# Kernel tuning notes

Measured on AMD Instinct MI355X. Metric: run time of the kernel, lower is better.

Reference implementation:

```python
import jax, jax.numpy as jnp
import numpy as np

B, N, K = 8, 2048, 4          # graphs per batch, nodes per graph, knn k
IN_CH, HID, C = 16, 128, 64   # in_channels, GCN hidden, n_clusters
E = 262144                    # input edges


def gcn_conv(x, src, dst, W, b):
    """PyG GCNConv: self-loops + symmetric normalization + linear."""
    n = x.shape[0]
    xw = x @ W
    loop = jnp.arange(n)
    s2 = jnp.concatenate([src, loop])
    d2 = jnp.concatenate([dst, loop])
    deg = jax.ops.segment_sum(jnp.ones(s2.shape[0], x.dtype), d2, num_segments=n)
    dis = jax.lax.rsqrt(deg)  # deg >= 1 thanks to self loops
    norm = dis[s2] * dis[d2]
    return jax.ops.segment_sum(xw[s2] * norm[:, None], d2, num_segments=n) + b


def knn_edges(coords):
    """knn_graph(k=K, loop=False) per graph; edges neighbor->node (source_to_target)."""
    c = coords.reshape(B, N, 3)
    d2 = jnp.sum((c[:, :, None, :] - c[:, None, :, :]) ** 2, -1)  # [B,N,N]
    d2 = d2 + jnp.eye(N, dtype=c.dtype) * jnp.asarray(1e10, c.dtype)  # exclude self
    _, idx = jax.lax.top_k(-d2, K)  # [B,N,K] local neighbor indices
    offs = (jnp.arange(B) * N)[:, None, None]
    src = (idx + offs).reshape(-1)
    dst = (jnp.broadcast_to(jnp.arange(N)[None, :, None], (B, N, K)) + offs).reshape(-1)
    return src, dst


def dmon_pool(x, adj, Wp, bp):
    """PyG DMoNPooling (eval mode, mask all-true since graphs are equal-sized)."""
    s = jax.nn.softmax(x @ Wp + bp, axis=-1)              # [B,N,C]
    out = jax.nn.selu(jnp.einsum('bnc,bnf->bcf', s, x))   # [B,C,F]
    out_adj = jnp.einsum('bnc,bnm,bmd->bcd', s, adj, s)   # [B,C,C]
    deg = adj.sum(1)                                      # column sums, [B,N]
    m = deg.sum(-1) / 2                                   # [B]
    ca = jnp.einsum('bnc,bn->bc', s, deg)                 # [B,C]
    normalizer = ca[:, :, None] * ca[:, None, :] / (2 * m)[:, None, None]
    spectral = (-jnp.trace(out_adj - normalizer, axis1=1, axis2=2) / (2 * m)).mean()
    ss = jnp.einsum('bnc,bnd->bcd', s, s)
    ss_fro = jnp.linalg.norm(ss, axis=(1, 2), keepdims=True)
    i_norm = jnp.sqrt(jnp.asarray(C, x.dtype))            # ||I_C||_F
    i_s = jnp.eye(C, dtype=x.dtype)
    ortho = jnp.linalg.norm(ss / ss_fro - i_s / i_norm, axis=(1, 2)).mean()
    cluster = (jnp.linalg.norm(s.sum(1), axis=1) / N * i_norm - 1).mean()
    return s, out, spectral, ortho, cluster


def forward(x, edge_src, edge_dst, W1, b1, W2, b2, Wp, bp):
    h = jax.nn.relu(gcn_conv(x, edge_src, edge_dst, W1, b1))
    src2, dst2 = knn_edges(h[:, :3])                      # dynamic graph on dims [0,1,2]
    h = jax.nn.relu(gcn_conv(h, src2, dst2, W2, b2))
    xd = h.reshape(B, N, HID)                             # to_dense_batch (equal-size graphs)
    g = edge_src // N                                     # to_dense_adj on ORIGINAL edges
    adj = jnp.zeros((B, N, N), x.dtype).at[g, edge_src % N, edge_dst % N].add(1.0)
    s, out, sp, o, cl = dmon_pool(xd, adj, Wp, bp)
    return jax.nn.log_softmax(out, axis=-1), sp + o + cl, s


def setup_inputs():
    key = jax.random.key(0)
    ks = jax.random.split(key, 8)
    x = jax.random.normal(ks[0], (B * N, IN_CH), jnp.float32)
    g = jax.random.randint(ks[1], (E,), 0, B)
    edge_src = (g * N + jax.random.randint(ks[2], (E,), 0, N)).astype(jnp.int32)
    edge_dst = (g * N + jax.random.randint(ks[3], (E,), 0, N)).astype(jnp.int32)
    batch = jnp.repeat(jnp.arange(B, dtype=jnp.int32), N)
    W1 = jax.random.normal(ks[4], (IN_CH, HID), jnp.float32) / np.sqrt(IN_CH)
    b1 = jnp.zeros((HID,), jnp.float32)
    W2 = jax.random.normal(ks[5], (HID, HID), jnp.float32) / np.sqrt(HID)
    b2 = jnp.zeros((HID,), jnp.float32)
    Wp = jax.random.normal(ks[6], (HID, C), jnp.float32) / np.sqrt(HID)
    bp = jnp.zeros((C,), jnp.float32)
    return {"x": x, "edge_src": edge_src, "edge_dst": edge_dst, "batch": batch,
            "W1": W1, "b1": b1, "W2": W2, "b2": b2, "Wp": Wp, "bp": bp}


def reference(x, edge_src, edge_dst, batch, W1, b1, W2, b2, Wp, bp):
    del batch  # graphs are equal-sized contiguous blocks of N nodes
    return forward(x, edge_src, edge_dst, W1, b1, W2, b2, Wp, bp)
```

## Files before the change

### kernel.cpp

```cpp
#include <hip/hip_runtime.h>
#include <math.h>

#define BGR 8
#define NN 2048
#define KNN 4
#define INCH 16
#define HID 128
#define CL 64
#define NE 262144
#define NT (BGR*NN)

#define OFF_CNT   0
#define OFF_CSR   16384
#define OFF_H1    1064960
#define OFF_NBR   3162112
#define OFF_SS    3227648
#define OFF_H2    4276224
#define OFF_TR    6373376
#define OFF_CA    6373384
#define OFF_SSUM  6373896
#define OFF_MS    6374408
#define OFF_H1C   6374416

__global__ void k_init(int* cnt, float* small, float* loss) {
  int i = blockIdx.x * 256 + threadIdx.x;
  if (i < 16384) cnt[i] = 0;
  int j = i - 16384;
  if (j >= 0 && j < 1040) small[j] = 0.f;
  if (i == 0) loss[0] = 0.f;
}

__global__ void k_bucket(const int* __restrict__ src, const int* __restrict__ dst,
                         int* __restrict__ cnt, int* __restrict__ csr) {
  int e = blockIdx.x * 256 + threadIdx.x;
  if (e >= NE) return;
  int d = dst[e];
  int slot = atomicAdd(&cnt[d], 1);
  if (slot < 64) csr[(d << 6) + slot] = src[e];
}

__global__ __launch_bounds__(256) void k_gemm1(const int* __restrict__ cnt,
    const int* __restrict__ csr, const float* __restrict__ x,
    const float* __restrict__ W1, const float* __restrict__ b1,
    float* __restrict__ h1, float* __restrict__ h1c) {
  __shared__ float a1[16][17];
  __shared__ float w[INCH * HID];
  __shared__ float disl[NN];
  int tid = threadIdx.x;
  int gbase = (blockIdx.x >> 7) * NN;
  for (int i = tid; i < NN; i += 256)
    disl[i] = rsqrtf((float)cnt[gbase + i] + 1.0f);
  for (int i = tid; i < INCH * HID / 4; i += 256) ((float4*)w)[i] = ((const float4*)W1)[i];
  int nl = tid >> 4, ch = tid & 15;
  int n = blockIdx.x * 16 + nl;
  int cnRaw = cnt[n];
  int cn = cnRaw > 64 ? 64 : cnRaw;
  const int* row = csr + (n << 6);
  __syncthreads();
  float dn = disl[n - gbase];
  float acc = 0.f;
  int sNext = (cn > 0) ? row[0] : 0;
  for (int e = 0; e < cn; e++) {
    int sc = sNext;
    if (e + 1 < cn) sNext = row[e + 1];
    acc += x[sc * INCH + ch] * disl[sc - gbase];
  }
  a1[nl][ch] = (acc + x[n * INCH + ch] * dn) * dn;
  __syncthreads();
  int j = tid & 127;
  int ng = (tid >> 7) * 8;
#pragma unroll
  for (int u = 0; u < 8; u++) {
    int node = ng + u;
    float s = b1[j];
#pragma unroll
    for (int c2 = 0; c2 < INCH; c2++) s += a1[node][c2] * w[c2 * HID + j];
    float v = fmaxf(s, 0.f);
    h1[(size_t)(blockIdx.x * 16 + node) * HID + j] = v;
    if (j < 4) h1c[(size_t)(blockIdx.x * 16 + node) * 4 + j] = v;
  }
}

__global__ __launch_bounds__(1024) void k_knn(const float* __restrict__ h1c, int* __restrict__ nbr) {
  __shared__ float4 c4[NN];
  int g = blockIdx.y, tid = threadIdx.x;
  const float4* src4 = (const float4*)h1c + (size_t)g * NN;
  for (int i = tid; i < NN; i += 1024) c4[i] = src4[i];
  __syncthreads();
  int wid = tid >> 6, lane = tid & 63;
  int row0 = blockIdx.x * 32 + wid * 2;
  float mx[2], my[2], mz[2];
#pragma unroll
  for (int r = 0; r < 2; r++) { float4 m = c4[row0 + r]; mx[r] = m.x; my[r] = m.y; mz[r] = m.z; }
  unsigned t0[2], t1[2], t2[2], t3[2];
#pragma unroll
  for (int r = 0; r < 2; r++) { t0[r] = t1[r] = t2[r] = t3[r] = 0xFFFFFFFFu; }
#pragma unroll 4
  for (int i = 0; i < 32; i++) {
    int j = i * 64 + lane;
    float4 p = c4[j];
#pragma unroll
    for (int r = 0; r < 2; r++) {
      float dx = p.x - mx[r], dy = p.y - my[r], dz = p.z - mz[r];
      float d2 = dx * dx + dy * dy + dz * dz;
      unsigned k = (__float_as_uint(d2) & 0xFFFFFFE0u) | (unsigned)i;
      if (j == row0 + r) k = 0xFFFFFFFFu;
      unsigned M0 = max(t0[r], k); t0[r] = min(t0[r], k);
      unsigned M1 = max(t1[r], M0); t1[r] = min(t1[r], M0);
      unsigned M2 = max(t2[r], M1); t2[r] = min(t2[r], M1);
      t3[r] = min(t3[r], M2);
    }
  }
#pragma unroll
  for (int r = 0; r < 2; r++) {
    unsigned a0 = t0[r], a1 = t1[r], a2 = t2[r], a3 = t3[r];
    int res[4];
#pragma unroll
    for (int k = 0; k < 4; k++) {
      int cj = (int)((a0 & 31u) << 6) | lane;
      unsigned wd = a0; int wj = cj;
#pragma unroll
      for (int off = 32; off; off >>= 1) {
        unsigned od = (unsigned)__shfl_xor((int)wd, off, 64);
        int oj = __shfl_xor(wj, off, 64);
        bool take = (od < wd) || (od == wd && oj < wj);
        wd = take ? od : wd; wj = take ? oj : wj;
      }
      res[k] = wj;
      bool pop = (cj == wj);
      a0 = pop ? a1 : a0; a1 = pop ? a2 : a1; a2 = pop ? a3 : a2;
      a3 = pop ? 0xFFFFFFFFu : a3;
    }
    if (lane == 0) {
      int node = g * NN + row0 + r;
      ((int4*)nbr)[node] = make_int4(g * NN + res[0], g * NN + res[1],
                                     g * NN + res[2], g * NN + res[3]);
    }
  }
}

__global__ __launch_bounds__(256) void k_gemm2s(const float* __restrict__ h1,
    const int* __restrict__ nbr, const float* __restrict__ W2,
    const float* __restrict__ b2, const float* __restrict__ Wp,
    const float* __restrict__ bp, float* __restrict__ h2,
    float* __restrict__ s_out) {
  __shared__ float smem[13344];
  float (*At)[33] = (float(*)[33])smem;
  float* Bt = smem + 1056;
  float (*H2t)[128] = (float(*)[128])smem;
  float* Wpl = smem + 5152;
  int tid = threadIdx.x;
  int bid = blockIdx.x;
  int rblock = (bid & 7) * 64 + (bid >> 3);
  int rbase = rblock * 32;
  int r = tid >> 3, q = tid & 7;
  int4 nb = ((const int4*)nbr)[rbase + r];
  const float4* h4 = (const float4*)h1;
  size_t r0 = (size_t)(rbase + r) * 32, rx = (size_t)nb.x * 32, ry = (size_t)nb.y * 32,
         rz = (size_t)nb.z * 32, rw = (size_t)nb.w * 32;
  int rg = tid >> 5;
  int cg = (tid & 31) * 4;
  float acc[4][4];
#pragma unroll
  for (int i = 0; i < 4; i++)
#pragma unroll
    for (int j = 0; j < 4; j++) acc[i][j] = 0.f;
  int kk = tid >> 5;
  int cc = (tid & 31) * 4;
  for (int k0 = 0; k0 < HID; k0 += 32) {
    {
      int q4 = (k0 >> 2) + q;
      float4 a = h4[r0 + q4], bx = h4[rx + q4], by = h4[ry + q4],
             bz = h4[rz + q4], bw = h4[rw + q4];
      int k = q * 4;
      At[r][k]     = (a.x + bx.x + by.x + bz.x + bw.x) * 0.2f;
      At[r][k + 1] = (a.y + bx.y + by.y + bz.y + bw.y) * 0.2f;
      At[r][k + 2] = (a.z + bx.z + by.z + bz.z + bw.z) * 0.2f;
      At[r][k + 3] = (a.w + bx.w + by.w + bz.w + bw.w) * 0.2f;
    }
#pragma unroll
    for (int u = 0; u < 4; u++)
      *(float4*)&Bt[(kk + u * 8) * 128 + cc] = *(const float4*)&W2[(k0 + kk + u * 8) * HID + cc];
    {
      int kt = k0 >> 5;
      *(float4*)&Wpl[kt * 2048 + tid * 8]     = *(const float4*)&Wp[kt * 2048 + tid * 8];
      *(float4*)&Wpl[kt * 2048 + tid * 8 + 4] = *(const float4*)&Wp[kt * 2048 + tid * 8 + 4];
    }
    __syncthreads();
#pragma unroll
    for (int k2 = 0; k2 < 32; k2++) {
      float4 bv = *(const float4*)&Bt[k2 * 128 + cg];
#pragma unroll
      for (int i = 0; i < 4; i++) {
        float av = At[rg * 4 + i][k2];
        acc[i][0] += av * bv.x; acc[i][1] += av * bv.y;
        acc[i][2] += av * bv.z; acc[i][3] += av * bv.w;
      }
    }
    __syncthreads();
  }
#pragma unroll
  for (int i = 0; i < 4; i++) {
    int rr = rbase + rg * 4 + i;
#pragma unroll
    for (int j = 0; j < 4; j++) {
      float v = acc[i][j] + b2[cg + j];
      v = fmaxf(v, 0.f);
      h2[(size_t)rr * HID + cg + j] = v;
      H2t[rg * 4 + i][cg + j] = v;
    }
  }
  __syncthreads();
  int c0 = (tid & 31) * 2;
  float acc2[4][2];
  float bp0 = bp[c0], bp1 = bp[c0 + 1];
#pragma unroll
  for (int i = 0; i < 4; i++) { acc2[i][0] = bp0; acc2[i][1] = bp1; }
#pragma unroll 4
  for (int k2 = 0; k2 < 128; k2++) {
    float w0 = Wpl[k2 * 64 + c0];
    float w1 = Wpl[k2 * 64 + c0 + 1];
#pragma unroll
    for (int i = 0; i < 4; i++) {
      float av = H2t[rg * 4 + i][k2];
      acc2[i][0] += av * w0; acc2[i][1] += av * w1;
    }
  }
#pragma unroll
  for (int i = 0; i < 4; i++) {
    float m = fmaxf(acc2[i][0], acc2[i][1]);
    for (int off = 1; off < 32; off <<= 1) m = fmaxf(m, __shfl_xor(m, off, 64));
    float e0 = expf(acc2[i][0] - m), e1 = expf(acc2[i][1] - m);
    float sum = e0 + e1;
    for (int off = 1; off < 32; off <<= 1) sum += __shfl_xor(sum, off, 64);
    float inv = 1.0f / sum;
    size_t o = (size_t)(rbase + rg * 4 + i) * CL + c0;
    s_out[o] = e0 * inv;
    s_out[o + 1] = e1 * inv;
  }
}

__global__ __launch_bounds__(256) void k_dmon_trace(const float* __restrict__ s,
    const float* __restrict__ h2, const int* __restrict__ cnt,
    float* __restrict__ part_pool, float* __restrict__ part_ss,
    float* __restrict__ ca, float* __restrict__ ssum, float* __restrict__ msum,
    const int* __restrict__ src, const int* __restrict__ dst, float* __restrict__ tr) {
  __shared__ float st[64 * 64];
  __shared__ float ht[64 * 128];
  __shared__ float dt[64];
  __shared__ float red[256];
  __shared__ float bins[8];
  int tid = threadIdx.x;
  if (blockIdx.x < 256) {
    int b = blockIdx.x & 7, sl = blockIdx.x >> 3;
    int nb = sl * 64;
    const float* sp = s + ((size_t)b * NN + nb) * CL;
    const float* hp = h2 + ((size_t)b * NN + nb) * HID;
    for (int i = tid; i < 64 * 64 / 4; i += 256) ((float4*)st)[i] = ((const float4*)sp)[i];
    for (int i = tid; i < 64 * 128 / 4; i += 256) ((float4*)ht)[i] = ((const float4*)hp)[i];
    if (tid < 64) dt[tid] = (float)cnt[b * NN + nb + tid];
    __syncthreads();
    int tc = tid & 15, tf = tid >> 4;
    int c0 = tc * 4, f0 = tf * 8;
    float pacc[4][8];
#pragma unroll
    for (int i = 0; i < 4; i++)
#pragma unroll
      for (int j = 0; j < 8; j++) pacc[i][j] = 0.f;
    for (int n = 0; n < 64; n++) {
      float4 sv = *(const float4*)&st[n * 64 + c0];
      float4 ha = *(const float4*)&ht[n * 128 + f0];
      float4 hb = *(const float4*)&ht[n * 128 + f0 + 4];
      float svv[4] = {sv.x, sv.y, sv.z, sv.w};
#pragma unroll
      for (int i = 0; i < 4; i++) {
        pacc[i][0] += svv[i] * ha.x; pacc[i][1] += svv[i] * ha.y;
        pacc[i][2] += svv[i] * ha.z; pacc[i][3] += svv[i] * ha.w;
        pacc[i][4] += svv[i] * hb.x; pacc[i][5] += svv[i] * hb.y;
        pacc[i][6] += svv[i] * hb.z; pacc[i][7] += svv[i] * hb.w;
      }
    }
    float* pp = part_pool + ((size_t)(b * 32 + sl)) * 8192;
#pragma unroll
    for (int i = 0; i < 4; i++) {
      *(float4*)&pp[(c0 + i) * 128 + f0]     = make_float4(pacc[i][0], pacc[i][1], pacc[i][2], pacc[i][3]);
      *(float4*)&pp[(c0 + i) * 128 + f0 + 4] = make_float4(pacc[i][4], pacc[i][5], pacc[i][6], pacc[i][7]);
    }
    int d0 = tf * 4;
    float sacc[4][4];
#pragma unroll
    for (int i = 0; i < 4; i++)
#pragma unroll
      for (int j = 0; j < 4; j++) sacc[i][j] = 0.f;
    for (int n = 0; n < 64; n++) {
      float4 a = *(const float4*)&st[n * 64 + c0];
      float4 bq = *(const float4*)&st[n * 64 + d0];
      float av[4] = {a.x, a.y, a.z, a.w};
#pragma unroll
      for (int i = 0; i < 4; i++) {
        sacc[i][0] += av[i] * bq.x; sacc[i][1] += av[i] * bq.y;
        sacc[i][2] += av[i] * bq.z; sacc[i][3] += av[i] * bq.w;
      }
    }
    float* ps = part_ss + ((size_t)(b * 32 + sl)) * 4096;
#pragma unroll
    for (int i = 0; i < 4; i++)
      *(float4*)&ps[(c0 + i) * 64 + d0] = make_float4(sacc[i][0], sacc[i][1], sacc[i][2], sacc[i][3]);
    int c = tid & 63;
    int q = tid >> 6;
    float a_ss = 0, a_ca = 0, a_m = 0;
    for (int n = q; n < 64; n += 4) {
      float sv = st[n * 64 + c];
      float dv = dt[n];
      a_ss += sv; a_ca += sv * dv;
      if (c == 0) a_m += dv;
    }
    red[tid] = a_ss; __syncthreads();
    if (q == 0) atomicAdd(&ssum[b * CL + c], red[c] + red[64 + c] + red[128 + c] + red[192 + c]);
    __syncthreads();
    red[tid] = a_ca; __syncthreads();
    if (q == 0) atomicAdd(&ca[b * CL + c], red[c] + red[64 + c] + red[128 + c] + red[192 + c]);
    __syncthreads();
    red[tid] = (c == 0) ? a_m : 0.f; __syncthreads();
    if (tid == 0) atomicAdd(&msum[b], red[0] + red[64] + red[128] + red[192]);
  } else {
    if (tid < 8) bins[tid] = 0.f;
    __syncthreads();
    int sub = tid & 15;
    int grp = ((blockIdx.x - 256) * 256 + tid) >> 4;
    const float4* s4 = (const float4*)s;
    for (int e = grp; e < NE; e += 8192) {
      int se = src[e], de = dst[e];
      float4 a = s4[se * 16 + sub];
      float4 b = s4[de * 16 + sub];
      float v = a.x * b.x + a.y * b.y + a.z * b.z + a.w * b.w;
      v += __shfl_xor(v, 1, 64);
      v += __shfl_xor(v, 2, 64);
      v += __shfl_xor(v, 4, 64);
      v += __shfl_xor(v, 8, 64);
      if (sub == 0) atomicAdd(&bins[se >> 11], v);
    }
    __syncthreads();
    if (tid < 8) atomicAdd(&tr[tid], bins[tid]);
  }
}

__global__ __launch_bounds__(256) void k_final(const float* __restrict__ part_pool,
    const float* __restrict__ part_ss, const float* __restrict__ ca,
    const float* __restrict__ ssum, const float* __restrict__ msum,
    const float* __restrict__ tr, float* __restrict__ out, float* __restrict__ outs) {
  int tid = threadIdx.x;
  if (blockIdx.x < 256) {
    __shared__ float r[4], r2[4];
    int half = tid >> 7, f = tid & 127;
    int row = blockIdx.x * 2 + half;
    int wid = tid >> 6;
    const float* p = part_pool + (size_t)(row >> 6) * 32 * 8192 + (row & 63) * 128 + f;
    float v = 0.f;
#pragma unroll
    for (int sl = 0; sl < 32; sl++) v += p[sl * 8192];
    const float scale = 1.0507009873554805f, alpha = 1.6732632423543772f;
    v = scale * (v > 0.f ? v : alpha * expm1f(v));
    float m = v;
    for (int off = 32; off; off >>= 1) m = fmaxf(m, __shfl_xor(m, off, 64));
    if ((tid & 63) == 0) r[wid] = m;
    __syncthreads();
    m = fmaxf(r[half * 2], r[half * 2 + 1]);
    float e = expf(v - m);
    float sum = e;
    for (int off = 32; off; off >>= 1) sum += __shfl_xor(sum, off, 64);
    if ((tid & 63) == 0) r2[wid] = sum;
    __syncthreads();
    sum = r2[half * 2] + r2[half * 2 + 1];
    out[(size_t)row * HID + f] = v - m - logf(sum);
  } else {
    __shared__ float ssb[4096];
    __shared__ float red[256];
    int b = blockIdx.x - 256;
    float loc = 0.f;
    for (int idx = tid; idx < 4096; idx += 256) {
      const float* p = part_ss + (size_t)b * 32 * 4096 + idx;
      float v = 0.f;
#pragma unroll
      for (int sl = 0; sl < 32; sl++) v += p[sl * 4096];
      ssb[idx] = v;
      loc += v * v;
    }
    red[tid] = loc; __syncthreads();
    for (int s2 = 128; s2; s2 >>= 1) { if (tid < s2) red[tid] += red[tid + s2]; __syncthreads(); }
    float fro = sqrtf(red[0]);
    __syncthreads();
    loc = 0.f;
    for (int i = tid; i < 4096; i += 256) {
      float v = ssb[i] / fro - (((i % 65) == 0) ? 0.125f : 0.f);
      loc += v * v;
    }
    red[tid] = loc; __syncthreads();
    for (int s2 = 128; s2; s2 >>= 1) { if (tid < s2) red[tid] += red[tid + s2]; __syncthreads(); }
    float ortho_b = sqrtf(red[0]);
    __syncthreads();
    loc = 0.f;
    if (tid < 64) { float v = ca[b * 64 + tid]; loc = v * v; }
    red[tid] = loc; __syncthreads();
    for (int s2 = 128; s2; s2 >>= 1) { if (tid < s2) red[tid] += red[tid + s2]; __syncthreads(); }
    float caSq = red[0];
    __syncthreads();
    loc = 0.f;
    if (tid < 64) { float v = ssum[b * 64 + tid]; loc = v * v; }
    red[tid] = loc; __syncthreads();
    for (int s2 = 128; s2; s2 >>= 1) { if (tid < s2) red[tid] += red[tid + s2]; __syncthreads(); }
    float ssumSq = red[0];
    __syncthreads();
    if (tid == 0) {
      float m2 = msum[b];
      float spectral_b = -(tr[b] - caSq / m2) / m2;
      float cluster_b = sqrtf(ssumSq) / 2048.0f * 8.0f - 1.0f;
      atomicAdd(&outs[0], (spectral_b + ortho_b + cluster_b) * 0.125f);
    }
  }
}

extern "C" void kernel_launch(void* const* d_in, const int* in_sizes, int n_in,
                              void* d_out, int out_size, void* d_ws, size_t ws_size,
                              hipStream_t stream) {
  (void)in_sizes; (void)n_in; (void)out_size; (void)ws_size;
  const float* x   = (const float*)d_in[0];
  const int* esrc  = (const int*)d_in[1];
  const int* edst  = (const int*)d_in[2];
  const float* W1  = (const float*)d_in[4];
  const float* b1  = (const float*)d_in[5];
  const float* W2  = (const float*)d_in[6];
  const float* b2  = (const float*)d_in[7];
  const float* Wp  = (const float*)d_in[8];
  const float* bp  = (const float*)d_in[9];
  float* out = (float*)d_out;
  float* ws  = (float*)d_ws;

  int*   cnt   = (int*)(ws + OFF_CNT);
  int*   csr   = (int*)(ws + OFF_CSR);
  float* h1    = ws + OFF_H1;
  int*   nbr   = (int*)(ws + OFF_NBR);
  float* h2    = ws + OFF_H2;
  float* tr    = ws + OFF_TR;
  float* ca    = ws + OFF_CA;
  float* ssum  = ws + OFF_SSUM;
  float* msum  = ws + OFF_MS;
  float* h1c   = ws + OFF_H1C;
  float* part_pool = ws + OFF_H1;
  float* part_ss   = ws + OFF_SS;
  float* s_out = out + 65537;

  k_init<<<69, 256, 0, stream>>>(cnt, ws + OFF_TR, out + 65536);
  k_bucket<<<NE / 256, 256, 0, stream>>>(esrc, edst, cnt, csr);
  k_gemm1<<<NT / 16, 256, 0, stream>>>(cnt, csr, x, W1, b1, h1, h1c);
  k_knn<<<dim3(64, 8), 1024, 0, stream>>>(h1c, nbr);
  k_gemm2s<<<NT / 32, 256, 0, stream>>>(h1, nbr, W2, b2, Wp, bp, h2, s_out);
  k_dmon_trace<<<768, 256, 0, stream>>>(s_out, h2, cnt, part_pool, part_ss,
                                        ca, ssum, msum, esrc, edst, tr);
  k_final<<<264, 256, 0, stream>>>(part_pool, part_ss, ca, ssum, msum, tr,
                                   out, out + 65536);
}
```

Before: 197.1 us.

## Fuse kNN search with GCN2 gemm and pooling softmax into one kernel

```diff
diff --git a/kernel.cpp b/kernel.cpp
--- a/kernel.cpp
+++ b/kernel.cpp
@@ -13,7 +13,6 @@
 #define OFF_CNT   0
 #define OFF_CSR   16384
 #define OFF_H1    1064960
-#define OFF_NBR   3162112
 #define OFF_SS    3227648
 #define OFF_H2    4276224
 #define OFF_TR    6373376
@@ -81,163 +80,135 @@
   }
 }
 
-__global__ __launch_bounds__(1024) void k_knn(const float* __restrict__ h1c, int* __restrict__ nbr) {
-  __shared__ float4 c4[NN];
-  int g = blockIdx.y, tid = threadIdx.x;
+__global__ __launch_bounds__(1024) void k_kgs(const float* __restrict__ h1,
+    const float* __restrict__ h1c, const float* __restrict__ W2,
+    const float* __restrict__ b2, const float* __restrict__ Wp,
+    const float* __restrict__ bp, float* __restrict__ h2,
+    float* __restrict__ s_out) {
+  __shared__ float smem[8448];
+  __shared__ int4 nbrL[32];
+  int tid = threadIdx.x;
+  int bid = blockIdx.x;
+  int g = bid & 7, lb = bid >> 3;
+  int rbase = g * NN + lb * 32;
+
+  float4* c4 = (float4*)smem;
   const float4* src4 = (const float4*)h1c + (size_t)g * NN;
   for (int i = tid; i < NN; i += 1024) c4[i] = src4[i];
   __syncthreads();
   int wid = tid >> 6, lane = tid & 63;
-  int row0 = blockIdx.x * 32 + wid * 2;
-  float mx[2], my[2], mz[2];
-#pragma unroll
-  for (int r = 0; r < 2; r++) { float4 m = c4[row0 + r]; mx[r] = m.x; my[r] = m.y; mz[r] = m.z; }
-  unsigned t0[2], t1[2], t2[2], t3[2];
-#pragma unroll
-  for (int r = 0; r < 2; r++) { t0[r] = t1[r] = t2[r] = t3[r] = 0xFFFFFFFFu; }
+  int row0 = lb * 32 + wid * 2;
+  {
+    float mx[2], my[2], mz[2];
+#pragma unroll
+    for (int r = 0; r < 2; r++) { float4 m = c4[row0 + r]; mx[r] = m.x; my[r] = m.y; mz[r] = m.z; }
+    unsigned t0[2], t1[2], t2[2], t3[2];
+#pragma unroll
+    for (int r = 0; r < 2; r++) { t0[r] = t1[r] = t2[r] = t3[r] = 0xFFFFFFFFu; }
 #pragma unroll 4
-  for (int i = 0; i < 32; i++) {
-    int j = i * 64 + lane;
-    float4 p = c4[j];
+    for (int i = 0; i < 32; i++) {
+      int j = i * 64 + lane;
+      float4 p = c4[j];
+#pragma unroll
+      for (int r = 0; r < 2; r++) {
+        float dx = p.x - mx[r], dy = p.y - my[r], dz = p.z - mz[r];
+        float d2 = dx * dx + dy * dy + dz * dz;
+        unsigned k = (__float_as_uint(d2) & 0xFFFFFFE0u) | (unsigned)i;
+        if (j == row0 + r) k = 0xFFFFFFFFu;
+        unsigned M0 = max(t0[r], k); t0[r] = min(t0[r], k);
+        unsigned M1 = max(t1[r], M0); t1[r] = min(t1[r], M0);
+        unsigned M2 = max(t2[r], M1); t2[r] = min(t2[r], M1);
+        t3[r] = min(t3[r], M2);
+      }
+    }
 #pragma unroll
     for (int r = 0; r < 2; r++) {
-      float dx = p.x - mx[r], dy = p.y - my[r], dz = p.z - mz[r];
-      float d2 = dx * dx + dy * dy + dz * dz;
-      unsigned k = (__float_as_uint(d2) & 0xFFFFFFE0u) | (unsigned)i;
-      if (j == row0 + r) k = 0xFFFFFFFFu;
-      unsigned M0 = max(t0[r], k); t0[r] = min(t0[r], k);
-      unsigned M1 = max(t1[r], M0); t1[r] = min(t1[r], M0);
-      unsigned M2 = max(t2[r], M1); t2[r] = min(t2[r], M1);
-      t3[r] = min(t3[r], M2);
-    }
-  }
-#pragma unroll
-  for (int r = 0; r < 2; r++) {
-    unsigned a0 = t0[r], a1 = t1[r], a2 = t2[r], a3 = t3[r];
-    int res[4];
-#pragma unroll
-    for (int k = 0; k < 4; k++) {
-      int cj = (int)((a0 & 31u) << 6) | lane;
-      unsigned wd = a0; int wj = cj;
-#pragma unroll
-      for (int off = 32; off; off >>= 1) {
-        unsigned od = (unsigned)__shfl_xor((int)wd, off, 64);
-        int oj = __shfl_xor(wj, off, 64);
-        bool take = (od < wd) || (od == wd && oj < wj);
-        wd = take ? od : wd; wj = take ? oj : wj;
+      unsigned a0 = t0[r], a1 = t1[r], a2 = t2[r], a3 = t3[r];
+      int res[4];
+#pragma unroll
+      for (int k = 0; k < 4; k++) {
+        int cj = (int)((a0 & 31u) << 6) | lane;
+        unsigned wd = a0; int wj = cj;
+#pragma unroll
+        for (int off = 32; off; off >>= 1) {
+          unsigned od = (unsigned)__shfl_xor((int)wd, off, 64);
+          int oj = __shfl_xor(wj, off, 64);
+          bool take = (od < wd) || (od == wd && oj < wj);
+          wd = take ? od : wd; wj = take ? oj : wj;
+        }
+        res[k] = wj;
+        bool pop = (cj == wj);
+        a0 = pop ? a1 : a0; a1 = pop ? a2 : a1; a2 = pop ? a3 : a2;
+        a3 = pop ? 0xFFFFFFFFu : a3;
       }
-      res[k] = wj;
-      bool pop = (cj == wj);
-      a0 = pop ? a1 : a0; a1 = pop ? a2 : a1; a2 = pop ? a3 : a2;
-      a3 = pop ? 0xFFFFFFFFu : a3;
-    }
-    if (lane == 0) {
-      int node = g * NN + row0 + r;
-      ((int4*)nbr)[node] = make_int4(g * NN + res[0], g * NN + res[1],
-                                     g * NN + res[2], g * NN + res[3]);
-    }
-  }
-}
-
-__global__ __launch_bounds__(256) void k_gemm2s(const float* __restrict__ h1,
-    const int* __restrict__ nbr, const float* __restrict__ W2,
-    const float* __restrict__ b2, const float* __restrict__ Wp,
-    const float* __restrict__ bp, float* __restrict__ h2,
-    float* __restrict__ s_out) {
-  __shared__ float smem[13344];
-  float (*At)[33] = (float(*)[33])smem;
-  float* Bt = smem + 1056;
+      if (lane == 0)
+        nbrL[wid * 2 + r] = make_int4(g * NN + res[0], g * NN + res[1],
+                                      g * NN + res[2], g * NN + res[3]);
+    }
+  }
+  __syncthreads();
+
+  float (*At)[132] = (float(*)[132])smem;
+  float* Bt = smem + 4224;
+  const float4* h4 = (const float4*)h1;
+  int row = tid >> 5, q = tid & 31;
+  {
+    int4 nb = nbrL[row];
+    size_t r0 = (size_t)(rbase + row) * 32;
+    float4 a  = h4[r0 + q];
+    float4 bx = h4[(size_t)nb.x * 32 + q];
+    float4 by = h4[(size_t)nb.y * 32 + q];
+    float4 bz = h4[(size_t)nb.z * 32 + q];
+    float4 bw = h4[(size_t)nb.w * 32 + q];
+    At[row][q * 4]     = (a.x + bx.x + by.x + bz.x + bw.x) * 0.2f;
+    At[row][q * 4 + 1] = (a.y + bx.y + by.y + bz.y + bw.y) * 0.2f;
+    At[row][q * 4 + 2] = (a.z + bx.z + by.z + bz.z + bw.z) * 0.2f;
+    At[row][q * 4 + 3] = (a.w + bx.w + by.w + bz.w + bw.w) * 0.2f;
+  }
+  int cg = q * 4;
+  float acc[4] = {0.f, 0.f, 0.f, 0.f};
+  for (int kt = 0; kt < 4; kt++) {
+    *(float4*)&Bt[row * 128 + cg] = *(const float4*)&W2[(kt * 32 + row) * HID + cg];
+    __syncthreads();
+#pragma unroll
+    for (int k2 = 0; k2 < 32; k2++) {
+      float av = At[row][kt * 32 + k2];
+      float4 bv = *(const float4*)&Bt[k2 * 128 + cg];
+      acc[0] += av * bv.x; acc[1] += av * bv.y;
+      acc[2] += av * bv.z; acc[3] += av * bv.w;
+    }
+    __syncthreads();
+  }
+  float4 b2v = *(const float4*)&b2[cg];
+  float4 hv = make_float4(fmaxf(acc[0] + b2v.x, 0.f), fmaxf(acc[1] + b2v.y, 0.f),
+                          fmaxf(acc[2] + b2v.z, 0.f), fmaxf(acc[3] + b2v.w, 0.f));
+  *(float4*)&h2[(size_t)(rbase + row) * HID + cg] = hv;
+
   float (*H2t)[128] = (float(*)[128])smem;
-  float* Wpl = smem + 5152;
-  int tid = threadIdx.x;
-  int bid = blockIdx.x;
-  int rblock = (bid & 7) * 64 + (bid >> 3);
-  int rbase = rblock * 32;
-  int r = tid >> 3, q = tid & 7;
-  int4 nb = ((const int4*)nbr)[rbase + r];
-  const float4* h4 = (const float4*)h1;
-  size_t r0 = (size_t)(rbase + r) * 32, rx = (size_t)nb.x * 32, ry = (size_t)nb.y * 32,
-         rz = (size_t)nb.z * 32, rw = (size_t)nb.w * 32;
-  int rg = tid >> 5;
-  int cg = (tid & 31) * 4;
-  float acc[4][4];
-#pragma unroll
-  for (int i = 0; i < 4; i++)
-#pragma unroll
-    for (int j = 0; j < 4; j++) acc[i][j] = 0.f;
-  int kk = tid >> 5;
-  int cc = (tid & 31) * 4;
-  for (int k0 = 0; k0 < HID; k0 += 32) {
-    {
-      int q4 = (k0 >> 2) + q;
-      float4 a = h4[r0 + q4], bx = h4[rx + q4], by = h4[ry + q4],
-             bz = h4[rz + q4], bw = h4[rw + q4];
-      int k = q * 4;
-      At[r][k]     = (a.x + bx.x + by.x + bz.x + bw.x) * 0.2f;
-      At[r][k + 1] = (a.y + bx.y + by.y + bz.y + bw.y) * 0.2f;
-      At[r][k + 2] = (a.z + bx.z + by.z + bz.z + bw.z) * 0.2f;
-      At[r][k + 3] = (a.w + bx.w + by.w + bz.w + bw.w) * 0.2f;
-    }
-#pragma unroll
-    for (int u = 0; u < 4; u++)
-      *(float4*)&Bt[(kk + u * 8) * 128 + cc] = *(const float4*)&W2[(k0 + kk + u * 8) * HID + cc];
-    {
-      int kt = k0 >> 5;
-      *(float4*)&Wpl[kt * 2048 + tid * 8]     = *(const float4*)&Wp[kt * 2048 + tid * 8];
-      *(float4*)&Wpl[kt * 2048 + tid * 8 + 4] = *(const float4*)&Wp[kt * 2048 + tid * 8 + 4];
-    }
+  float* Wt = smem + 4096;
+  *(float4*)&H2t[row][cg] = hv;
+  int c0 = q * 2;
+  float acc2[2] = {bp[c0], bp[c0 + 1]};
+  for (int kt = 0; kt < 4; kt++) {
+    if (tid < 512) *(float4*)&Wt[tid * 4] = *(const float4*)&Wp[kt * 2048 + tid * 4];
     __syncthreads();
 #pragma unroll
     for (int k2 = 0; k2 < 32; k2++) {
-      float4 bv = *(const float4*)&Bt[k2 * 128 + cg];
-#pragma unroll
-      for (int i = 0; i < 4; i++) {
-        float av = At[rg * 4 + i][k2];
-        acc[i][0] += av * bv.x; acc[i][1] += av * bv.y;
-        acc[i][2] += av * bv.z; acc[i][3] += av * bv.w;
-      }
-    }
-    __syncthreads();
-  }
-#pragma unroll
-  for (int i = 0; i < 4; i++) {
-    int rr = rbase + rg * 4 + i;
-#pragma unroll
-    for (int j = 0; j < 4; j++) {
-      float v = acc[i][j] + b2[cg + j];
-      v = fmaxf(v, 0.f);
-      h2[(size_t)rr * HID + cg + j] = v;
-      H2t[rg * 4 + i][cg + j] = v;
-    }
-  }
-  __syncthreads();
-  int c0 = (tid & 31) * 2;
-  float acc2[4][2];
-  float bp0 = bp[c0], bp1 = bp[c0 + 1];
-#pragma unroll
-  for (int i = 0; i < 4; i++) { acc2[i][0] = bp0; acc2[i][1] = bp1; }
-#pragma unroll 4
-  for (int k2 = 0; k2 < 128; k2++) {
-    float w0 = Wpl[k2 * 64 + c0];
-    float w1 = Wpl[k2 * 64 + c0 + 1];
-#pragma unroll
-    for (int i = 0; i < 4; i++) {
-      float av = H2t[rg * 4 + i][k2];
-      acc2[i][0] += av * w0; acc2[i][1] += av * w1;
-    }
-  }
-#pragma unroll
-  for (int i = 0; i < 4; i++) {
-    float m = fmaxf(acc2[i][0], acc2[i][1]);
-    for (int off = 1; off < 32; off <<= 1) m = fmaxf(m, __shfl_xor(m, off, 64));
-    float e0 = expf(acc2[i][0] - m), e1 = expf(acc2[i][1] - m);
-    float sum = e0 + e1;
-    for (int off = 1; off < 32; off <<= 1) sum += __shfl_xor(sum, off, 64);
-    float inv = 1.0f / sum;
-    size_t o = (size_t)(rbase + rg * 4 + i) * CL + c0;
-    s_out[o] = e0 * inv;
-    s_out[o + 1] = e1 * inv;
-  }
+      float av = H2t[row][kt * 32 + k2];
+      acc2[0] += av * Wt[k2 * 64 + c0];
+      acc2[1] += av * Wt[k2 * 64 + c0 + 1];
+    }
+    __syncthreads();
+  }
+  float m = fmaxf(acc2[0], acc2[1]);
+  for (int off = 1; off < 32; off <<= 1) m = fmaxf(m, __shfl_xor(m, off, 64));
+  float e0 = expf(acc2[0] - m), e1 = expf(acc2[1] - m);
+  float sum = e0 + e1;
+  for (int off = 1; off < 32; off <<= 1) sum += __shfl_xor(sum, off, 64);
+  float inv = 1.0f / sum;
+  size_t o = (size_t)(rbase + row) * CL + c0;
+  s_out[o] = e0 * inv;
+  s_out[o + 1] = e1 * inv;
 }
 
 __global__ __launch_bounds__(256) void k_dmon_trace(const float* __restrict__ s,
@@ -439,7 +410,6 @@
   int*   cnt   = (int*)(ws + OFF_CNT);
   int*   csr   = (int*)(ws + OFF_CSR);
   float* h1    = ws + OFF_H1;
-  int*   nbr   = (int*)(ws + OFF_NBR);
   float* h2    = ws + OFF_H2;
   float* tr    = ws + OFF_TR;
   float* ca    = ws + OFF_CA;
@@ -453,8 +423,7 @@
   k_init<<<69, 256, 0, stream>>>(cnt, ws + OFF_TR, out + 65536);
   k_bucket<<<NE / 256, 256, 0, stream>>>(esrc, edst, cnt, csr);
   k_gemm1<<<NT / 16, 256, 0, stream>>>(cnt, csr, x, W1, b1, h1, h1c);
-  k_knn<<<dim3(64, 8), 1024, 0, stream>>>(h1c, nbr);
-  k_gemm2s<<<NT / 32, 256, 0, stream>>>(h1, nbr, W2, b2, Wp, bp, h2, s_out);
+  k_kgs<<<512, 1024, 0, stream>>>(h1, h1c, W2, b2, Wp, bp, h2, s_out);
   k_dmon_trace<<<768, 256, 0, stream>>>(s_out, h2, cnt, part_pool, part_ss,
                                         ca, ssum, msum, esrc, edst, tr);
   k_final<<<264, 256, 0, stream>>>(part_pool, part_ss, ca, ssum, msum, tr,
```

New measurement: 451.6 us. 129% more time.
